# Performance work log

Measured on AMD Instinct MI355X. Metric: run time of the kernel, lower is better.

## Reference

```python
import jax, jax.numpy as jnp
import numpy as np

N_QUBITS = 12
N_LAYERS = 3
N_PARAMS = N_QUBITS * 3 * N_LAYERS  # 108
BATCH = 8192
DIM = 1 << N_QUBITS  # 4096


def _rx(theta):
    c = jnp.cos(theta / 2).astype(jnp.complex64)
    s = jnp.sin(theta / 2).astype(jnp.complex64)
    return jnp.stack([jnp.stack([c, -1j * s]), jnp.stack([-1j * s, c])])


def _ry(theta):
    c = jnp.cos(theta / 2).astype(jnp.complex64)
    s = jnp.sin(theta / 2).astype(jnp.complex64)
    return jnp.stack([jnp.stack([c, -s]), jnp.stack([s, c])])


def _rz(theta):
    e = jnp.exp(-1j * theta.astype(jnp.complex64) / 2)
    z = jnp.zeros((), jnp.complex64)
    return jnp.stack([jnp.stack([e, z]), jnp.stack([z, jnp.conj(e)])])


def _apply_1q(state, q, U):
    # state: (B,) + (2,)*n ; apply 2x2 gate U on wire q (axis q+1)
    s = jnp.moveaxis(state, q + 1, -1)
    s = s @ U.T
    return jnp.moveaxis(s, -1, q + 1)


def _cnot(state, c, t):
    # control wire c, target wire t (axes offset by 1 for batch dim)
    ca, ta = c + 1, t + 1
    s0 = jax.lax.index_in_dim(state, 0, ca, keepdims=False)
    s1 = jax.lax.index_in_dim(state, 1, ca, keepdims=False)
    ta2 = ta - 1 if ta > ca else ta  # target axis shifts after removing control axis
    s1 = jnp.flip(s1, axis=ta2)  # X on target (size-2 axis)
    return jnp.stack([s0, s1], axis=ca)


def setup_inputs() -> dict:
    key = jax.random.key(0)
    k1, k2 = jax.random.split(key)
    x = jax.random.normal(k1, (BATCH, DIM), dtype=jnp.float32)
    params = jax.random.normal(k2, (N_PARAMS,), dtype=jnp.float32) * 0.1
    return {"x": x, "params": params}


def reference(x, params):
    n = N_QUBITS
    B = x.shape[0]
    # AmplitudeEmbedding with normalize=True
    norm = jnp.linalg.norm(x, axis=1, keepdims=True)
    state = (x / norm).astype(jnp.complex64).reshape((B,) + (2,) * n)
    idx = 0
    for _ in range(N_LAYERS):
        for q in range(n):
            state = _apply_1q(state, q, _rx(params[idx])); idx += 1
            state = _apply_1q(state, q, _ry(params[idx])); idx += 1
            state = _apply_1q(state, q, _rz(params[idx])); idx += 1
        for q in range(n):
            state = _cnot(state, q, (q + 1) % n)
    # <Z_q> = P(q=0) - P(q=1)
    p = state.real ** 2 + state.imag ** 2  # (B,) + (2,)*n, float32
    outs = []
    for q in range(n):
        axes = tuple(a for a in range(1, n + 1) if a != q + 1)
        marg = jnp.sum(p, axis=axes)  # (B, 2)
        outs.append(marg[:, 0] - marg[:, 1])
    return jnp.stack(outs, axis=1)  # (B, n_qubits)
```

## Files before the change

### kernel.cpp

```cpp
#include <hip/hip_runtime.h>
#include <math.h>

#define NQ 12
#define DIM 4096
#define NGATES 36
#define NROUND 9

typedef float f32x4 __attribute__((ext_vector_type(4)));
typedef __fp16 fp16x2 __attribute__((ext_vector_type(2)));
typedef __fp16 fp16x4 __attribute__((ext_vector_type(4)));
typedef __fp16 fp16x8 __attribute__((ext_vector_type(8)));

constexpr unsigned swz(unsigned x) { return x ^ (x >> 4); }

struct Round {
  unsigned s[4];
  unsigned l[4];
  unsigned cbsw8[16];
  unsigned dt[4];
};
struct PlanT {
  Round rd[NROUND];
  unsigned zsel[NQ];
};

constexpr PlanT make_plan() {
  PlanT P{};
  unsigned Mcol[NQ] = {}, Minv[NQ] = {};
  for (int i = 0; i < NQ; ++i) { Mcol[i] = 1u << i; Minv[i] = 1u << i; }
  unsigned gm[NGATES] = {}, gs[NGATES] = {};
  int g = 0;
  for (int L = 0; L < 3; ++L) {
    for (int q = 0; q < NQ; ++q) { int b = NQ - 1 - q; gm[g] = Mcol[b]; gs[g] = Minv[b]; ++g; }
    for (int q = 0; q < NQ; ++q) {
      int bc = NQ - 1 - q, bt = NQ - 1 - ((q + 1) % NQ);
      Mcol[bc] ^= Mcol[bt];
      Minv[bt] ^= Minv[bc];
    }
  }
  for (int r = 0; r < NROUND; ++r) {
    unsigned m[4], red[4];
    for (int k = 0; k < 4; ++k) { m[k] = gm[4*r+k]; red[k] = m[k]; P.rd[r].s[k] = gs[4*r+k]; }
    for (int a = 0; a < 4; ++a) {
      unsigned p = red[a] & (0u - red[a]);
      for (int b = a + 1; b < 4; ++b) if (red[b] & p) red[b] ^= red[a];
    }
    unsigned piv[4];
    for (int a = 0; a < 4; ++a) piv[a] = red[a] & (0u - red[a]);
    for (int a = 0; a < 4; ++a)
      for (int b = a + 1; b < 4; ++b)
        if (piv[a] > piv[b]) { unsigned tp = piv[a]; piv[a] = piv[b]; piv[b] = tp; }
    for (int a = 0; a < 4; ++a) P.rd[r].l[a] = piv[a] - 1u;
    for (int d = 0; d < 16; ++d) {
      unsigned c = 0;
      for (int k = 0; k < 4; ++k) if (d & (1 << k)) c ^= m[k];
      P.rd[r].cbsw8[d] = swz(c) << 3;
    }
    for (int tt = 0; tt < 4; ++tt) {
      unsigned c = (unsigned)tt << 4;
      unsigned j = c;
      j = ((j & ~P.rd[r].l[0]) << 1) | (j & P.rd[r].l[0]);
      j = ((j & ~P.rd[r].l[1]) << 1) | (j & P.rd[r].l[1]);
      j = ((j & ~P.rd[r].l[2]) << 1) | (j & P.rd[r].l[2]);
      j = ((j & ~P.rd[r].l[3]) << 1) | (j & P.rd[r].l[3]);
      unsigned d = swz(j) << 3;
      for (int k = 0; k < 4; ++k)
        if (__builtin_popcount(j & P.rd[r].s[k]) & 1) d ^= P.rd[r].cbsw8[1u << k];
      P.rd[r].dt[tt] = d;
    }
  }
  for (int q = 0; q < NQ; ++q) P.zsel[q] = Minv[NQ - 1 - q];
  return P;
}

constexpr PlanT PLAN = make_plan();

__global__ void qc_prep(const float* __restrict__ params, __fp16* __restrict__ amat) {
  int t = threadIdx.x;
  int r = t >> 4, s = t & 15;
  if (r >= NROUND) return;
  float U[4][8];
  for (int k = 0; k < 4; ++k) {
    int gg = r * 4 + k;
    float h1 = params[3*gg+0]*0.5f, hh2 = params[3*gg+1]*0.5f, h3 = params[3*gg+2]*0.5f;
    float c1 = cosf(h1), s1 = sinf(h1);
    float c2 = cosf(hh2), s2 = sinf(hh2);
    float c3 = cosf(h3), s3 = sinf(h3);
    float a00r =  c2*c1, a00i =  s2*s1;
    float a01r = -s2*c1, a01i = -c2*s1;
    float a10r =  s2*c1, a10i = -c2*s1;
    float a11r =  c2*c1, a11i = -s2*s1;
    U[k][0] = c3*a00r + s3*a00i;  U[k][1] = c3*a00i - s3*a00r;
    U[k][2] = c3*a01r + s3*a01i;  U[k][3] = c3*a01i - s3*a01r;
    U[k][4] = c3*a10r - s3*a10i;  U[k][5] = c3*a10i + s3*a10r;
    U[k][6] = c3*a11r - s3*a11i;  U[k][7] = c3*a11i + s3*a11r;
  }
  __fp16* b0 = amat + r*2048 + s*32;
  __fp16* b1 = b0 + 512;
  __fp16* b2 = b0 + 1024;
  __fp16* b3 = b0 + 1536;
  for (int j = 0; j < 16; ++j) {
    float pr = 1.f, pi = 0.f;
    for (int k = 0; k < 4; ++k) {
      int idx = ((((s >> k) & 1) * 2) + ((j >> k) & 1)) * 2;
      float gr = U[k][idx], gi = U[k][idx + 1];
      float npr = pr * gr - pi * gi;
      pi = pr * gi + pi * gr;
      pr = npr;
    }
    float v0_ =  pr; __fp16 e0 = (__fp16)v0_;
    float v1_ = -pi; __fp16 e1 = (__fp16)v1_;
    float v2_ =  pi; __fp16 e2 = (__fp16)v2_;
    float v3_ =  pr; __fp16 e3 = (__fp16)v3_;
    b0[2*j]   = e0;  b1[2*j]   = (__fp16)(v0_ - (float)e0);
    b0[2*j+1] = e1;  b1[2*j+1] = (__fp16)(v1_ - (float)e1);
    b2[2*j]   = e2;  b3[2*j]   = (__fp16)(v2_ - (float)e2);
    b2[2*j+1] = e3;  b3[2*j+1] = (__fp16)(v3_ - (float)e3);
  }
}

__global__ __launch_bounds__(256)
__attribute__((amdgpu_waves_per_eu(4, 5)))
void qc_main(const float* __restrict__ x, const __fp16* __restrict__ amat,
             float* __restrict__ out) {
  __shared__ float2 sst[DIM];
  char* sb = (char*)sst;
  const int t = threadIdx.x;
  const long row = blockIdx.x;

  const float4* x4 = (const float4*)(x + (size_t)row * DIM);
  float ssq = 0.f;
#pragma unroll
  for (int k = 0; k < 4; ++k) {
    float4 a = x4[t + 256*k];
    int j0 = 4*(t + 256*k);
    *(float2*)(sb + (swz((unsigned)j0)     << 3)) = make_float2(a.x, 0.f);
    *(float2*)(sb + (swz((unsigned)(j0+1)) << 3)) = make_float2(a.y, 0.f);
    *(float2*)(sb + (swz((unsigned)(j0+2)) << 3)) = make_float2(a.z, 0.f);
    *(float2*)(sb + (swz((unsigned)(j0+3)) << 3)) = make_float2(a.w, 0.f);
    ssq += a.x*a.x + a.y*a.y + a.z*a.z + a.w*a.w;
  }
#pragma unroll
  for (int off = 32; off > 0; off >>= 1) ssq += __shfl_down(ssq, off, 64);
  __syncthreads();

#pragma unroll 1
  for (int r = 0; r < NROUND; ++r) {
    const unsigned s0 = PLAN.rd[r].s[0], sA = PLAN.rd[r].s[1];
    const unsigned sB = PLAN.rd[r].s[2], sC = PLAN.rd[r].s[3];
    const unsigned l0 = PLAN.rd[r].l[0], l1 = PLAN.rd[r].l[1];
    const unsigned l2 = PLAN.rd[r].l[2], l3 = PLAN.rd[r].l[3];
    const unsigned CB1 = PLAN.rd[r].cbsw8[1], CB2 = PLAN.rd[r].cbsw8[2];
    const unsigned CB3 = PLAN.rd[r].cbsw8[3];
    const unsigned C4 = PLAN.rd[r].cbsw8[4], C8 = PLAN.rd[r].cbsw8[8];
    const unsigned dts[4] = {0u, PLAN.rd[r].dt[1], PLAN.rd[r].dt[2], PLAN.rd[r].dt[3]};

    unsigned j = ((unsigned)t & 0xC0u) | ((unsigned)t & 15u);
    j = ((j & ~l0) << 1) | (j & l0);
    j = ((j & ~l1) << 1) | (j & l1);
    j = ((j & ~l2) << 1) | (j & l2);
    j = ((j & ~l3) << 1) | (j & l3);
    unsigned adj8 = 0;
    adj8 ^= (unsigned)(-(int)(__popc(j & s0) & 1)) & CB1;
    adj8 ^= (unsigned)(-(int)(__popc(j & sA) & 1)) & CB2;
    adj8 ^= (unsigned)(-(int)(__popc(j & sB) & 1)) & C4;
    adj8 ^= (unsigned)(-(int)(__popc(j & sC) & 1)) & C8;
    const unsigned q = ((unsigned)t >> 4) & 3u;
    const unsigned qsel = ((q & 1u) ? C4 : 0u) ^ ((q & 2u) ? C8 : 0u);
    const unsigned b0a = (((j ^ (j >> 4)) << 3) ^ adj8) ^ qsel;

    const fp16x8* am = (const fp16x8*)(amat + (size_t)r * 2048);
    const int fo = (t & 15) * 4 + (int)q;
    const fp16x8 Arh = am[fo];
    const fp16x8 Arl = am[64 + fo];
    const fp16x8 Aih = am[128 + fo];
    const fp16x8 Ail = am[192 + fo];

    unsigned ad[4];
    float2 A[4][4];
#pragma unroll
    for (int tt = 0; tt < 4; ++tt) {
      const unsigned bb = b0a ^ dts[tt];
      ad[tt] = bb;
      A[tt][0] = *(const float2*)(sb + bb);
      A[tt][1] = *(const float2*)(sb + (bb ^ CB1));
      A[tt][2] = *(const float2*)(sb + (bb ^ CB2));
      A[tt][3] = *(const float2*)(sb + (bb ^ CB3));
    }

    fp16x8 Bhi[4], Blo[4];
#pragma unroll
    for (int tt = 0; tt < 4; ++tt) {
      fp16x2 p0 = __builtin_amdgcn_cvt_pkrtz(A[tt][0].x, A[tt][0].y);
      fp16x2 p1 = __builtin_amdgcn_cvt_pkrtz(A[tt][1].x, A[tt][1].y);
      fp16x2 p2 = __builtin_amdgcn_cvt_pkrtz(A[tt][2].x, A[tt][2].y);
      fp16x2 p3 = __builtin_amdgcn_cvt_pkrtz(A[tt][3].x, A[tt][3].y);
      fp16x2 q0 = __builtin_amdgcn_cvt_pkrtz(A[tt][0].x - (float)p0[0], A[tt][0].y - (float)p0[1]);
      fp16x2 q1 = __builtin_amdgcn_cvt_pkrtz(A[tt][1].x - (float)p1[0], A[tt][1].y - (float)p1[1]);
      fp16x2 q2 = __builtin_amdgcn_cvt_pkrtz(A[tt][2].x - (float)p2[0], A[tt][2].y - (float)p2[1]);
      fp16x2 q3 = __builtin_amdgcn_cvt_pkrtz(A[tt][3].x - (float)p3[0], A[tt][3].y - (float)p3[1]);
      fp16x4 u01 = __builtin_shufflevector(p0, p1, 0, 1, 2, 3);
      fp16x4 u23 = __builtin_shufflevector(p2, p3, 0, 1, 2, 3);
      Bhi[tt] = __builtin_shufflevector(u01, u23, 0, 1, 2, 3, 4, 5, 6, 7);
      fp16x4 w01 = __builtin_shufflevector(q0, q1, 0, 1, 2, 3);
      fp16x4 w23 = __builtin_shufflevector(q2, q3, 0, 1, 2, 3);
      Blo[tt] = __builtin_shufflevector(w01, w23, 0, 1, 2, 3, 4, 5, 6, 7);
    }

    f32x4 are[4], aim[4];
#pragma unroll
    for (int tt = 0; tt < 4; ++tt) {
      are[tt] = (f32x4){0.f, 0.f, 0.f, 0.f};
      aim[tt] = (f32x4){0.f, 0.f, 0.f, 0.f};
      are[tt] = __builtin_amdgcn_mfma_f32_16x16x32_f16(Arh, Bhi[tt], are[tt], 0, 0, 0);
      aim[tt] = __builtin_amdgcn_mfma_f32_16x16x32_f16(Aih, Bhi[tt], aim[tt], 0, 0, 0);
      are[tt] = __builtin_amdgcn_mfma_f32_16x16x32_f16(Arl, Bhi[tt], are[tt], 0, 0, 0);
      aim[tt] = __builtin_amdgcn_mfma_f32_16x16x32_f16(Ail, Bhi[tt], aim[tt], 0, 0, 0);
      are[tt] = __builtin_amdgcn_mfma_f32_16x16x32_f16(Arh, Blo[tt], are[tt], 0, 0, 0);
      aim[tt] = __builtin_amdgcn_mfma_f32_16x16x32_f16(Aih, Blo[tt], aim[tt], 0, 0, 0);
    }

#pragma unroll
    for (int tt = 0; tt < 4; ++tt) {
      *(float2*)(sb + ad[tt])         = make_float2(are[tt][0], aim[tt][0]);
      *(float2*)(sb + (ad[tt] ^ CB1)) = make_float2(are[tt][1], aim[tt][1]);
      *(float2*)(sb + (ad[tt] ^ CB2)) = make_float2(are[tt][2], aim[tt][2]);
      *(float2*)(sb + (ad[tt] ^ CB3)) = make_float2(are[tt][3], aim[tt][3]);
    }
    __syncthreads();
  }

  const unsigned mbase8 = (((16u * (unsigned)t) ^ (unsigned)t) << 3);
  float p[16];
#pragma unroll
  for (int c = 0; c < 16; ++c) {
    float2 v = *(const float2*)(sb + (mbase8 ^ ((unsigned)c << 3)));
    p[c] = v.x * v.x + v.y * v.y;
  }
#pragma unroll
  for (int b = 0; b < 4; ++b) {
#pragma unroll
    for (int c = 0; c < 16; ++c) {
      if (!(c & (1 << b))) {
        const int c1 = c | (1 << b);
        float u = p[c], v = p[c1];
        p[c] = u + v; p[c1] = u - v;
      }
    }
  }
  float zs[NQ];
#pragma unroll
  for (int qq = 0; qq < NQ; ++qq) {
    const unsigned m = PLAN.zsel[qq];
    const float v = p[m & 15u];
    const int sgn = __popc((unsigned)t & (m >> 4)) & 1;
    zs[qq] = sgn ? -v : v;
  }

  __syncthreads();
#pragma unroll
  for (int k = 0; k < 6; ++k)
    *(float2*)(sb + (((unsigned)(k << 8) + (unsigned)t) << 3)) =
        make_float2(zs[2*k], zs[2*k+1]);
  if ((t & 63) == 0) *(float*)(sb + 12288 + (t >> 6) * 4) = ssq;
  __syncthreads();
  if (t < 192) {
    const int k = t >> 5, j = t & 31;
    const char* cbp = sb + (k << 11) + (j << 3);
    float2 acc = *(const float2*)(cbp);
#pragma unroll
    for (int i = 1; i < 8; ++i) {
      float2 vv = *(const float2*)(cbp + i * 256);
      acc.x += vv.x; acc.y += vv.y;
    }
#pragma unroll
    for (int off = 16; off > 0; off >>= 1) {
      acc.x += __shfl_down(acc.x, off, 32);
      acc.y += __shfl_down(acc.y, off, 32);
    }
    if (j == 0) *(float2*)(sb + 12352 + (k << 3)) = acc;
  }
  __syncthreads();
  if (t < NQ) {
    const float* sq = (const float*)(sb + 12288);
    const float den = sq[0] + sq[1] + sq[2] + sq[3];
    out[row * NQ + t] = ((const float*)(sb + 12352))[t] / den;
  }
}

extern "C" void kernel_launch(void* const* d_in, const int* in_sizes, int n_in,
                              void* d_out, int out_size, void* d_ws, size_t ws_size,
                              hipStream_t stream) {
  const float* x = (const float*)d_in[0];
  const float* params = (const float*)d_in[1];
  float* out = (float*)d_out;
  __fp16* amat = (__fp16*)d_ws;
  const int nrows = in_sizes[0] / DIM;
  qc_prep<<<dim3(1), dim3(256), 0, stream>>>(params, amat);
  qc_main<<<dim3(nrows), dim3(256), 0, stream>>>(x, amat, out);
}
```

Measured before the change: 306.8 us.

## Process two batch rows per block to share gate matrices and barriers

Each block now handles two state vectors held in a doubled shared-memory buffer. Per round, the fp16 gate-matrix fragments and address math are loaded and computed once and used by interleaved MFMAs on both rows, which halves the per-row cost of plan loads, index computation and __syncthreads. The tile loop is restructured to load, convert, multiply and store per tile rather than in separate phases. Shared memory per block doubles to 64KB and the waves-per-EU hint drops to 2, which lowers occupancy and the latency hiding that comes with it.

```diff
diff --git a/kernel.cpp b/kernel.cpp
--- a/kernel.cpp
+++ b/kernel.cpp
@@ -119,29 +119,60 @@
   }
 }
 
+__device__ __forceinline__ void mk_b(const float2* A, fp16x8& hi, fp16x8& lo) {
+  fp16x2 p0 = __builtin_amdgcn_cvt_pkrtz(A[0].x, A[0].y);
+  fp16x2 p1 = __builtin_amdgcn_cvt_pkrtz(A[1].x, A[1].y);
+  fp16x2 p2 = __builtin_amdgcn_cvt_pkrtz(A[2].x, A[2].y);
+  fp16x2 p3 = __builtin_amdgcn_cvt_pkrtz(A[3].x, A[3].y);
+  fp16x2 q0 = __builtin_amdgcn_cvt_pkrtz(A[0].x - (float)p0[0], A[0].y - (float)p0[1]);
+  fp16x2 q1 = __builtin_amdgcn_cvt_pkrtz(A[1].x - (float)p1[0], A[1].y - (float)p1[1]);
+  fp16x2 q2 = __builtin_amdgcn_cvt_pkrtz(A[2].x - (float)p2[0], A[2].y - (float)p2[1]);
+  fp16x2 q3 = __builtin_amdgcn_cvt_pkrtz(A[3].x - (float)p3[0], A[3].y - (float)p3[1]);
+  fp16x4 u01 = __builtin_shufflevector(p0, p1, 0, 1, 2, 3);
+  fp16x4 u23 = __builtin_shufflevector(p2, p3, 0, 1, 2, 3);
+  hi = __builtin_shufflevector(u01, u23, 0, 1, 2, 3, 4, 5, 6, 7);
+  fp16x4 w01 = __builtin_shufflevector(q0, q1, 0, 1, 2, 3);
+  fp16x4 w23 = __builtin_shufflevector(q2, q3, 0, 1, 2, 3);
+  lo = __builtin_shufflevector(w01, w23, 0, 1, 2, 3, 4, 5, 6, 7);
+}
+
 __global__ __launch_bounds__(256)
-__attribute__((amdgpu_waves_per_eu(4, 5)))
+__attribute__((amdgpu_waves_per_eu(2)))
 void qc_main(const float* __restrict__ x, const __fp16* __restrict__ amat,
              float* __restrict__ out) {
-  __shared__ float2 sst[DIM];
+  __shared__ float2 sst[2 * DIM];
   char* sb = (char*)sst;
   const int t = threadIdx.x;
-  const long row = blockIdx.x;
-
-  const float4* x4 = (const float4*)(x + (size_t)row * DIM);
-  float ssq = 0.f;
+  const long rp = blockIdx.x;
+
+  const float4* x40 = (const float4*)(x + (size_t)(2 * rp) * DIM);
+  const float4* x41 = (const float4*)(x + (size_t)(2 * rp + 1) * DIM);
+  float ssq0 = 0.f, ssq1 = 0.f;
 #pragma unroll
   for (int k = 0; k < 4; ++k) {
-    float4 a = x4[t + 256*k];
+    float4 a = x40[t + 256*k];
+    float4 b = x41[t + 256*k];
     int j0 = 4*(t + 256*k);
-    *(float2*)(sb + (swz((unsigned)j0)     << 3)) = make_float2(a.x, 0.f);
-    *(float2*)(sb + (swz((unsigned)(j0+1)) << 3)) = make_float2(a.y, 0.f);
-    *(float2*)(sb + (swz((unsigned)(j0+2)) << 3)) = make_float2(a.z, 0.f);
-    *(float2*)(sb + (swz((unsigned)(j0+3)) << 3)) = make_float2(a.w, 0.f);
-    ssq += a.x*a.x + a.y*a.y + a.z*a.z + a.w*a.w;
-  }
-#pragma unroll
-  for (int off = 32; off > 0; off >>= 1) ssq += __shfl_down(ssq, off, 64);
+    unsigned o0 = swz((unsigned)j0)     << 3;
+    unsigned o1 = swz((unsigned)(j0+1)) << 3;
+    unsigned o2 = swz((unsigned)(j0+2)) << 3;
+    unsigned o3 = swz((unsigned)(j0+3)) << 3;
+    *(float2*)(sb + o0) = make_float2(a.x, 0.f);
+    *(float2*)(sb + o1) = make_float2(a.y, 0.f);
+    *(float2*)(sb + o2) = make_float2(a.z, 0.f);
+    *(float2*)(sb + o3) = make_float2(a.w, 0.f);
+    *(float2*)(sb + (o0 | 0x8000u)) = make_float2(b.x, 0.f);
+    *(float2*)(sb + (o1 | 0x8000u)) = make_float2(b.y, 0.f);
+    *(float2*)(sb + (o2 | 0x8000u)) = make_float2(b.z, 0.f);
+    *(float2*)(sb + (o3 | 0x8000u)) = make_float2(b.w, 0.f);
+    ssq0 += a.x*a.x + a.y*a.y + a.z*a.z + a.w*a.w;
+    ssq1 += b.x*b.x + b.y*b.y + b.z*b.z + b.w*b.w;
+  }
+#pragma unroll
+  for (int off = 32; off > 0; off >>= 1) {
+    ssq0 += __shfl_down(ssq0, off, 64);
+    ssq1 += __shfl_down(ssq1, off, 64);
+  }
   __syncthreads();
 
 #pragma unroll 1
@@ -176,115 +207,121 @@
     const fp16x8 Aih = am[128 + fo];
     const fp16x8 Ail = am[192 + fo];
 
-    unsigned ad[4];
-    float2 A[4][4];
 #pragma unroll
     for (int tt = 0; tt < 4; ++tt) {
       const unsigned bb = b0a ^ dts[tt];
-      ad[tt] = bb;
-      A[tt][0] = *(const float2*)(sb + bb);
-      A[tt][1] = *(const float2*)(sb + (bb ^ CB1));
-      A[tt][2] = *(const float2*)(sb + (bb ^ CB2));
-      A[tt][3] = *(const float2*)(sb + (bb ^ CB3));
-    }
-
-    fp16x8 Bhi[4], Blo[4];
-#pragma unroll
-    for (int tt = 0; tt < 4; ++tt) {
-      fp16x2 p0 = __builtin_amdgcn_cvt_pkrtz(A[tt][0].x, A[tt][0].y);
-      fp16x2 p1 = __builtin_amdgcn_cvt_pkrtz(A[tt][1].x, A[tt][1].y);
-      fp16x2 p2 = __builtin_amdgcn_cvt_pkrtz(A[tt][2].x, A[tt][2].y);
-      fp16x2 p3 = __builtin_amdgcn_cvt_pkrtz(A[tt][3].x, A[tt][3].y);
-      fp16x2 q0 = __builtin_amdgcn_cvt_pkrtz(A[tt][0].x - (float)p0[0], A[tt][0].y - (float)p0[1]);
-      fp16x2 q1 = __builtin_amdgcn_cvt_pkrtz(A[tt][1].x - (float)p1[0], A[tt][1].y - (float)p1[1]);
-      fp16x2 q2 = __builtin_amdgcn_cvt_pkrtz(A[tt][2].x - (float)p2[0], A[tt][2].y - (float)p2[1]);
-      fp16x2 q3 = __builtin_amdgcn_cvt_pkrtz(A[tt][3].x - (float)p3[0], A[tt][3].y - (float)p3[1]);
-      fp16x4 u01 = __builtin_shufflevector(p0, p1, 0, 1, 2, 3);
-      fp16x4 u23 = __builtin_shufflevector(p2, p3, 0, 1, 2, 3);
-      Bhi[tt] = __builtin_shufflevector(u01, u23, 0, 1, 2, 3, 4, 5, 6, 7);
-      fp16x4 w01 = __builtin_shufflevector(q0, q1, 0, 1, 2, 3);
-      fp16x4 w23 = __builtin_shufflevector(q2, q3, 0, 1, 2, 3);
-      Blo[tt] = __builtin_shufflevector(w01, w23, 0, 1, 2, 3, 4, 5, 6, 7);
-    }
-
-    f32x4 are[4], aim[4];
-#pragma unroll
-    for (int tt = 0; tt < 4; ++tt) {
-      are[tt] = (f32x4){0.f, 0.f, 0.f, 0.f};
-      aim[tt] = (f32x4){0.f, 0.f, 0.f, 0.f};
-      are[tt] = __builtin_amdgcn_mfma_f32_16x16x32_f16(Arh, Bhi[tt], are[tt], 0, 0, 0);
-      aim[tt] = __builtin_amdgcn_mfma_f32_16x16x32_f16(Aih, Bhi[tt], aim[tt], 0, 0, 0);
-      are[tt] = __builtin_amdgcn_mfma_f32_16x16x32_f16(Arl, Bhi[tt], are[tt], 0, 0, 0);
-      aim[tt] = __builtin_amdgcn_mfma_f32_16x16x32_f16(Ail, Bhi[tt], aim[tt], 0, 0, 0);
-      are[tt] = __builtin_amdgcn_mfma_f32_16x16x32_f16(Arh, Blo[tt], are[tt], 0, 0, 0);
-      aim[tt] = __builtin_amdgcn_mfma_f32_16x16x32_f16(Aih, Blo[tt], aim[tt], 0, 0, 0);
-    }
-
-#pragma unroll
-    for (int tt = 0; tt < 4; ++tt) {
-      *(float2*)(sb + ad[tt])         = make_float2(are[tt][0], aim[tt][0]);
-      *(float2*)(sb + (ad[tt] ^ CB1)) = make_float2(are[tt][1], aim[tt][1]);
-      *(float2*)(sb + (ad[tt] ^ CB2)) = make_float2(are[tt][2], aim[tt][2]);
-      *(float2*)(sb + (ad[tt] ^ CB3)) = make_float2(are[tt][3], aim[tt][3]);
+      const unsigned a0 = bb, a1 = bb ^ CB1, a2 = bb ^ CB2, a3 = bb ^ CB3;
+      float2 A0[4], A1[4];
+      A0[0] = *(const float2*)(sb + a0);
+      A0[1] = *(const float2*)(sb + a1);
+      A0[2] = *(const float2*)(sb + a2);
+      A0[3] = *(const float2*)(sb + a3);
+      A1[0] = *(const float2*)(sb + (a0 | 0x8000u));
+      A1[1] = *(const float2*)(sb + (a1 | 0x8000u));
+      A1[2] = *(const float2*)(sb + (a2 | 0x8000u));
+      A1[3] = *(const float2*)(sb + (a3 | 0x8000u));
+      fp16x8 Bh0, Bl0, Bh1, Bl1;
+      mk_b(A0, Bh0, Bl0);
+      mk_b(A1, Bh1, Bl1);
+
+      f32x4 re0 = {0.f,0.f,0.f,0.f}, im0 = {0.f,0.f,0.f,0.f};
+      f32x4 re1 = {0.f,0.f,0.f,0.f}, im1 = {0.f,0.f,0.f,0.f};
+      re0 = __builtin_amdgcn_mfma_f32_16x16x32_f16(Arh, Bh0, re0, 0, 0, 0);
+      re1 = __builtin_amdgcn_mfma_f32_16x16x32_f16(Arh, Bh1, re1, 0, 0, 0);
+      im0 = __builtin_amdgcn_mfma_f32_16x16x32_f16(Aih, Bh0, im0, 0, 0, 0);
+      im1 = __builtin_amdgcn_mfma_f32_16x16x32_f16(Aih, Bh1, im1, 0, 0, 0);
+      re0 = __builtin_amdgcn_mfma_f32_16x16x32_f16(Arl, Bh0, re0, 0, 0, 0);
+      re1 = __builtin_amdgcn_mfma_f32_16x16x32_f16(Arl, Bh1, re1, 0, 0, 0);
+      im0 = __builtin_amdgcn_mfma_f32_16x16x32_f16(Ail, Bh0, im0, 0, 0, 0);
+      im1 = __builtin_amdgcn_mfma_f32_16x16x32_f16(Ail, Bh1, im1, 0, 0, 0);
+      re0 = __builtin_amdgcn_mfma_f32_16x16x32_f16(Arh, Bl0, re0, 0, 0, 0);
+      re1 = __builtin_amdgcn_mfma_f32_16x16x32_f16(Arh, Bl1, re1, 0, 0, 0);
+      im0 = __builtin_amdgcn_mfma_f32_16x16x32_f16(Aih, Bl0, im0, 0, 0, 0);
+      im1 = __builtin_amdgcn_mfma_f32_16x16x32_f16(Aih, Bl1, im1, 0, 0, 0);
+
+      *(float2*)(sb + a0) = make_float2(re0[0], im0[0]);
+      *(float2*)(sb + a1) = make_float2(re0[1], im0[1]);
+      *(float2*)(sb + a2) = make_float2(re0[2], im0[2]);
+      *(float2*)(sb + a3) = make_float2(re0[3], im0[3]);
+      *(float2*)(sb + (a0 | 0x8000u)) = make_float2(re1[0], im1[0]);
+      *(float2*)(sb + (a1 | 0x8000u)) = make_float2(re1[1], im1[1]);
+      *(float2*)(sb + (a2 | 0x8000u)) = make_float2(re1[2], im1[2]);
+      *(float2*)(sb + (a3 | 0x8000u)) = make_float2(re1[3], im1[3]);
     }
     __syncthreads();
   }
 
   const unsigned mbase8 = (((16u * (unsigned)t) ^ (unsigned)t) << 3);
-  float p[16];
-#pragma unroll
-  for (int c = 0; c < 16; ++c) {
-    float2 v = *(const float2*)(sb + (mbase8 ^ ((unsigned)c << 3)));
-    p[c] = v.x * v.x + v.y * v.y;
-  }
-#pragma unroll
-  for (int b = 0; b < 4; ++b) {
+  float zs[2][NQ];
+#pragma unroll
+  for (int rr = 0; rr < 2; ++rr) {
+    const char* base = sb + (rr << 15);
+    float p[16];
 #pragma unroll
     for (int c = 0; c < 16; ++c) {
-      if (!(c & (1 << b))) {
-        const int c1 = c | (1 << b);
-        float u = p[c], v = p[c1];
-        p[c] = u + v; p[c1] = u - v;
+      float2 v = *(const float2*)(base + (mbase8 ^ ((unsigned)c << 3)));
+      p[c] = v.x * v.x + v.y * v.y;
+    }
+#pragma unroll
+    for (int b = 0; b < 4; ++b) {
+#pragma unroll
+      for (int c = 0; c < 16; ++c) {
+        if (!(c & (1 << b))) {
+          const int c1 = c | (1 << b);
+          float u = p[c], v = p[c1];
+          p[c] = u + v; p[c1] = u - v;
+        }
       }
     }
-  }
-  float zs[NQ];
-#pragma unroll
-  for (int qq = 0; qq < NQ; ++qq) {
-    const unsigned m = PLAN.zsel[qq];
-    const float v = p[m & 15u];
-    const int sgn = __popc((unsigned)t & (m >> 4)) & 1;
-    zs[qq] = sgn ? -v : v;
+#pragma unroll
+    for (int qq = 0; qq < NQ; ++qq) {
+      const unsigned m = PLAN.zsel[qq];
+      const float v = p[m & 15u];
+      const int sgn = __popc((unsigned)t & (m >> 4)) & 1;
+      zs[rr][qq] = sgn ? -v : v;
+    }
   }
 
   __syncthreads();
 #pragma unroll
-  for (int k = 0; k < 6; ++k)
-    *(float2*)(sb + (((unsigned)(k << 8) + (unsigned)t) << 3)) =
-        make_float2(zs[2*k], zs[2*k+1]);
-  if ((t & 63) == 0) *(float*)(sb + 12288 + (t >> 6) * 4) = ssq;
+  for (int rr = 0; rr < 2; ++rr) {
+    char* base = sb + (rr << 15);
+#pragma unroll
+    for (int k = 0; k < 6; ++k)
+      *(float2*)(base + (((unsigned)(k << 8) + (unsigned)t) << 3)) =
+          make_float2(zs[rr][2*k], zs[rr][2*k+1]);
+    if ((t & 63) == 0) *(float*)(base + 12288 + (t >> 6) * 4) = rr ? ssq1 : ssq0;
+  }
   __syncthreads();
-  if (t < 192) {
-    const int k = t >> 5, j = t & 31;
-    const char* cbp = sb + (k << 11) + (j << 3);
-    float2 acc = *(const float2*)(cbp);
-#pragma unroll
-    for (int i = 1; i < 8; ++i) {
-      float2 vv = *(const float2*)(cbp + i * 256);
-      acc.x += vv.x; acc.y += vv.y;
-    }
-#pragma unroll
-    for (int off = 16; off > 0; off >>= 1) {
-      acc.x += __shfl_down(acc.x, off, 32);
-      acc.y += __shfl_down(acc.y, off, 32);
-    }
-    if (j == 0) *(float2*)(sb + 12352 + (k << 3)) = acc;
+#pragma unroll
+  for (int rr = 0; rr < 2; ++rr) {
+    char* base = sb + (rr << 15);
+    if (t < 192) {
+      const int k = t >> 5, jj = t & 31;
+      const char* cbp = base + (k << 11) + (jj << 3);
+      float2 acc = *(const float2*)(cbp);
+#pragma unroll
+      for (int i = 1; i < 8; ++i) {
+        float2 vv = *(const float2*)(cbp + i * 256);
+        acc.x += vv.x; acc.y += vv.y;
+      }
+#pragma unroll
+      for (int off = 16; off > 0; off >>= 1) {
+        acc.x += __shfl_down(acc.x, off, 32);
+        acc.y += __shfl_down(acc.y, off, 32);
+      }
+      if (jj == 0) *(float2*)(base + 12352 + (k << 3)) = acc;
+    }
   }
   __syncthreads();
   if (t < NQ) {
-    const float* sq = (const float*)(sb + 12288);
-    const float den = sq[0] + sq[1] + sq[2] + sq[3];
-    out[row * NQ + t] = ((const float*)(sb + 12352))[t] / den;
+#pragma unroll
+    for (int rr = 0; rr < 2; ++rr) {
+      const char* base = sb + (rr << 15);
+      const float* sq = (const float*)(base + 12288);
+      const float den = sq[0] + sq[1] + sq[2] + sq[3];
+      out[(2 * rp + rr) * NQ + t] = ((const float*)(base + 12352))[t] / den;
+    }
   }
 }
 
@@ -297,5 +334,5 @@
   __fp16* amat = (__fp16*)d_ws;
   const int nrows = in_sizes[0] / DIM;
   qc_prep<<<dim3(1), dim3(256), 0, stream>>>(params, amat);
-  qc_main<<<dim3(nrows), dim3(256), 0, stream>>>(x, amat, out);
-}
+  qc_main<<<dim3(nrows / 2), dim3(256), 0, stream>>>(x, amat, out);
+}
```

Measured after the change: 325.2 us. 1.06x slower.
